# Kernel tuning notes

Measured on AMD Instinct MI355X. Metric: run time of the kernel, lower is better.

The kernel has to match this reference:

```python
import jax, jax.numpy as jnp
import numpy as np

D_MODEL = 128
N_HEADS = 8
RES_SCALE = 2.0 ** (-0.5)  # self_normalizing residual scale

OCC = np.array([65,66,67,68,69,70,71,72,73,74,75,76,77,81,82,83,84,88,89,90,94], dtype=np.int64)


def conv1d_same(x, w, groups=1):
    # x: [B, Cin, T], w: [Cout, Cin//groups, K] -> [B, Cout, T], 'same' padding, no bias
    return jax.lax.conv_general_dilated(
        x, w, window_strides=(1,), padding='SAME',
        dimension_numbers=('NCH', 'OIH', 'NCH'),
        feature_group_count=groups)


def setup_inputs() -> dict:
    key = jax.random.key(0)
    ks = jax.random.split(key, 7)
    B, C, T = 8, 128, 500
    L, D, O, K = 2, D_MODEL, 21, 9
    def lecun(k, shape, fan_in):
        return jax.random.normal(k, shape, dtype=jnp.float32) / jnp.sqrt(jnp.float32(fan_in))
    return {
        'x': jax.random.normal(ks[0], (B, C, T), dtype=jnp.float32),
        'occ_idx': jnp.asarray(OCC),
        'wq': lecun(ks[1], (L, D, O, K), O * K),
        'wk': lecun(ks[2], (L, C * D, 1, K), K),
        'wv': lecun(ks[3], (L, C * D, 1, K), K),
        'wproj': lecun(ks[4], (L, C, D), D),
        'w_head': lecun(ks[5], (40, C * T), C * T),
        'b_head': jnp.zeros((40,), dtype=jnp.float32),
    }


def reference(x, occ_idx, wq, wk, wv, wproj, w_head, b_head):
    B, C, T = x.shape
    L = wq.shape[0]
    H, D = N_HEADS, D_MODEL
    d = D // H  # head dim
    scale = d ** (-0.5)
    selu = jax.nn.selu
    for l in range(L):
        x_occ = x[:, occ_idx]                               # [B, O, T]
        Q = selu(conv1d_same(x_occ, wq[l]))                 # [B, D, T]
        K = selu(conv1d_same(x, wk[l], groups=C))           # [B, C*D, T]
        V = selu(conv1d_same(x, wv[l], groups=C))           # [B, C*D, T]
        Qh = Q.reshape(B, H, d, T)                          # b (h d) t -> b h d t
        Kh = K.reshape(B, C, H, d, T).transpose(0, 2, 1, 3, 4)  # b h c d t
        Vh = V.reshape(B, C, H, d, T).transpose(0, 2, 1, 3, 4)
        gates = selu(jnp.einsum('bhdt,bhcdt->bhct', Qh, Kh) * scale)
        out = jnp.einsum('bhct,bhcdt->bhcdt', gates, Vh)    # [B, H, C, d, T]
        out = out.transpose(0, 2, 1, 3, 4).reshape(B, C, D, T)  # b (c h d) t grouped by c
        # grouped 1x1 conv (groups=C): per-channel projection D -> 1
        out = selu(jnp.einsum('bcdt,cd->bct', out, wproj[l]))
        x = (x + out) * RES_SCALE
    logits = x.reshape(B, -1) @ w_head.T + b_head           # [B, n_classes]
    return logits
```

## Files before the change

kernel.cpp:

```cpp
#include <hip/hip_runtime.h>
#include <math.h>

#define T_LEN   500
#define C_CH    128
#define DM      128
#define N_OCC   21
#define KSZ     9
#define N_OUT   40
#define LOG2E   1.44269504088896340736f

typedef _Float16 f16x8 __attribute__((ext_vector_type(8)));
typedef float    f32x16 __attribute__((ext_vector_type(16)));

__device__ __forceinline__ float exp2_fast(float y) {
#if __has_builtin(__builtin_amdgcn_exp2f)
    return __builtin_amdgcn_exp2f(y);
#else
    return exp2f(y);
#endif
}

__device__ __forceinline__ float selu2(float y) {
    const float c1 = 0.7282904300f;
    const float la = 1.7580993408473766f;
    float e = exp2_fast(y);
    return y > 0.f ? c1 * y : fmaf(la, e, -la);
}

__global__ void wq_transpose(const float* __restrict__ wq, float* __restrict__ wqT) {
    int idx = blockIdx.x * 256 + threadIdx.x;
    if (idx >= 2 * N_OCC * KSZ * DM) return;
    int D  = idx & 127;
    int r  = idx >> 7;
    int k  = r % KSZ;
    int r2 = r / KSZ;
    int o  = r2 % N_OCC;
    int l  = r2 / N_OCC;
    wqT[idx] = wq[(((size_t)l * DM + D) * N_OCC + o) * KSZ + k] * LOG2E;
}

__global__ void wprep_kernel(const float* __restrict__ wk, const float* __restrict__ wv,
                             _Float16* __restrict__ wkh, _Float16* __restrict__ wvh)
{
    int idx = blockIdx.x * 256 + threadIdx.x;
    if (idx >= 2 * C_CH * 4 * 64) return;
    int lane = idx & 63;
    int ch   = (idx >> 6) & 3;
    int c    = (idx >> 8) & 127;
    int l    = idx >> 15;
    int tcol = lane & 31, hi = lane >> 5;
    int D    = ch * 32 + tcol;
    const float* wkp = wk + ((size_t)l * C_CH * DM + (size_t)c * DM + D) * KSZ;
    const float* wvp = wv + ((size_t)l * C_CH * DM + (size_t)c * DM + D) * KSZ;
#pragma unroll
    for (int j = 0; j < 8; ++j) {
        int k = 8 * hi + j;
        wkh[(size_t)idx * 8 + j] = (k < KSZ) ? (_Float16)(wkp[k] * LOG2E) : (_Float16)0.f;
        wvh[(size_t)idx * 8 + j] = (k < KSZ) ? (_Float16)(wvp[k] * LOG2E) : (_Float16)0.f;
    }
}

#define ATCH 4
__global__ __launch_bounds__(128) void qconv_kernel(
    const float* __restrict__ xin, const int* __restrict__ occ,
    const float* __restrict__ wqT, float* __restrict__ qtT2, int l)
{
    const int b  = blockIdx.y;
    const int t0 = blockIdx.x * ATCH;
    const int D  = threadIdx.x;
    __shared__ float xo[N_OCC][ATCH + 8];
    for (int i = threadIdx.x; i < N_OCC * (ATCH + 8); i += 128) {
        int o = i / (ATCH + 8), j = i % (ATCH + 8);
        int tg = t0 + j - 4;
        xo[o][j] = (tg >= 0 && tg < T_LEN)
                     ? xin[((size_t)b * C_CH + occ[o]) * T_LEN + tg] : 0.f;
    }
    __syncthreads();

    float acc[ATCH];
#pragma unroll
    for (int tt = 0; tt < ATCH; ++tt) acc[tt] = 0.f;

    for (int o = 0; o < N_OCC; ++o) {
        float xr[ATCH + 8];
#pragma unroll
        for (int j = 0; j < ATCH + 8; ++j) xr[j] = xo[o][j];
#pragma unroll
        for (int k = 0; k < KSZ; ++k) {
            float w = wqT[(((size_t)l * N_OCC + o) * KSZ + k) * DM + D];
#pragma unroll
            for (int tt = 0; tt < ATCH; ++tt)
                acc[tt] = fmaf(xr[tt + k], w, acc[tt]);
        }
    }
    float4 st;
#pragma unroll
    for (int tt = 0; tt < ATCH; ++tt) (&st.x)[tt] = selu2(acc[tt]);
    const int tile = t0 >> 5, tl = t0 & 31;
    *reinterpret_cast<float4*>(
        &qtT2[((size_t)(b * 16 + tile) * DM + D) * 32 + tl]) = st;
}

__global__ __launch_bounds__(256) void fused_layer(
    const float* __restrict__ xin, const float* __restrict__ qtT2,
    const f16x8* __restrict__ wkh, const f16x8* __restrict__ wvh,
    const float* __restrict__ wproj, float* __restrict__ xout, int l)
{
    const int c = blockIdx.x, b = blockIdx.y, zi = blockIdx.z;
    const int tid  = threadIdx.x;
    const int wave = tid >> 6;
    const int lane = tid & 63;
    const int tcol = lane & 31;
    const int hi   = lane >> 5;

    __shared__ float xs[272];
    const float* xp = xin + ((size_t)(b * C_CH + c)) * T_LEN;
    for (int i = tid; i < 272; i += 256) {
        int tg = zi * 256 + i - 4;
        xs[i] = (tg >= 0 && tg < T_LEN) ? xp[tg] : 0.f;
    }
    __syncthreads();

    const f16x8* wkf = wkh + ((size_t)(l * C_CH + c) * 4) * 64 + lane;
    const f16x8* wvf = wvh + ((size_t)(l * C_CH + c) * 4) * 64 + lane;
    f16x8 ak[4], av[4];
#pragma unroll
    for (int ch = 0; ch < 4; ++ch) {
        ak[ch] = wkf[ch * 64];
        av[ch] = wvf[ch * 64];
    }

    const float4* wp4p = reinterpret_cast<const float4*>(
        wproj + ((size_t)l * C_CH + c) * DM);

#pragma unroll 1
    for (int ti = 0; ti < 2; ++ti) {
        const int loc0 = wave * 64 + ti * 32;
        const int tile = zi * 8 + wave * 2 + ti;
        const int t    = zi * 256 + loc0 + tcol;

        f16x8 bfr;
        {
            const int base = loc0 + tcol + 8 * hi;
#pragma unroll
            for (int j = 0; j < 8; ++j) bfr[j] = (_Float16)xs[base + j];
        }

        float qk[8];
#pragma unroll
        for (int h = 0; h < 8; ++h) qk[h] = 0.f;

#pragma unroll
        for (int ch = 0; ch < 4; ++ch) {
            const float* qTp = qtT2
                + ((size_t)(b * 16 + tile) * DM + ch * 32 + 4 * hi) * 32 + tcol;
            float qv[16];
#pragma unroll
            for (int I = 0; I < 4; ++I)
#pragma unroll
                for (int i2 = 0; i2 < 4; ++i2)
                    qv[4 * I + i2] = qTp[(8 * I + i2) * 32];

            f32x16 acc;
#pragma unroll
            for (int j = 0; j < 16; ++j) acc[j] = 0.f;
            acc = __builtin_amdgcn_mfma_f32_32x32x16_f16(ak[ch], bfr, acc, 0, 0, 0);

            float pA = 0.f, pB = 0.f;
#pragma unroll
            for (int I = 0; I < 4; ++I) {
#pragma unroll
                for (int i2 = 0; i2 < 4; ++i2) {
                    float kv = selu2(acc[4 * I + i2]);
                    float qvv = qv[4 * I + i2];
                    if (I < 2) pA = fmaf(qvv, kv, pA);
                    else       pB = fmaf(qvv, kv, pB);
                }
            }
            qk[ch * 2 + 0] += pA;
            qk[ch * 2 + 1] += pB;
        }

        float g[8];
#pragma unroll
        for (int h = 0; h < 8; ++h) {
            float full = qk[h] + __shfl_xor(qk[h], 32);
            g[h] = selu2(full * (0.25f * LOG2E));
        }

        float outp = 0.f;
#pragma unroll
        for (int ch = 0; ch < 4; ++ch) {
            f32x16 acc;
#pragma unroll
            for (int j = 0; j < 16; ++j) acc[j] = 0.f;
            acc = __builtin_amdgcn_mfma_f32_32x32x16_f16(av[ch], bfr, acc, 0, 0, 0);
            float sA = 0.f, sB = 0.f;
#pragma unroll
            for (int I = 0; I < 4; ++I) {
                float4 wq4 = wp4p[ch * 8 + 2 * I + hi];
#pragma unroll
                for (int i2 = 0; i2 < 4; ++i2) {
                    float vv = selu2(acc[4 * I + i2]);
                    if (I < 2) sA = fmaf((&wq4.x)[i2], vv, sA);
                    else       sB = fmaf((&wq4.x)[i2], vv, sB);
                }
            }
            outp = fmaf(g[ch * 2 + 0], sA, outp);
            outp = fmaf(g[ch * 2 + 1], sB, outp);
        }
        float outf = outp + __shfl_xor(outp, 32);

        if (hi == 0 && t < T_LEN) {
            const float rs = 0.70710678118654752f;
            xout[((size_t)(b * C_CH + c)) * T_LEN + t]
                = (xs[loc0 + tcol + 4] + selu2(outf * LOG2E)) * rs;
        }
    }
}

#define NCHUNK 8
#define CHUNK  (C_CH * T_LEN / NCHUNK)
__global__ __launch_bounds__(256) void head_partial(
    const float* __restrict__ x, const float* __restrict__ wh,
    float* __restrict__ part)
{
    const int o  = blockIdx.x;
    const int ch = blockIdx.y;
    const int base = ch * CHUNK;
    const float4* wp = reinterpret_cast<const float4*>(wh + (size_t)o * (C_CH * T_LEN) + base);

    float acc[8];
#pragma unroll
    for (int b = 0; b < 8; ++b) acc[b] = 0.f;

    for (int i = threadIdx.x; i < CHUNK / 4; i += 256) {
        float4 w4 = wp[i];
#pragma unroll
        for (int b = 0; b < 8; ++b) {
            float4 x4 = reinterpret_cast<const float4*>(
                x + (size_t)b * (C_CH * T_LEN) + base)[i];
            acc[b] = fmaf(x4.x, w4.x, acc[b]);
            acc[b] = fmaf(x4.y, w4.y, acc[b]);
            acc[b] = fmaf(x4.z, w4.z, acc[b]);
            acc[b] = fmaf(x4.w, w4.w, acc[b]);
        }
    }

#pragma unroll
    for (int b = 0; b < 8; ++b)
#pragma unroll
        for (int off = 32; off > 0; off >>= 1)
            acc[b] += __shfl_down(acc[b], off);

    __shared__ float red[4][8];
    const int lane = threadIdx.x & 63, wid = threadIdx.x >> 6;
    if (lane == 0)
#pragma unroll
        for (int b = 0; b < 8; ++b) red[wid][b] = acc[b];
    __syncthreads();
    if (threadIdx.x < 8) {
        int b = threadIdx.x;
        part[((size_t)o * NCHUNK + ch) * 8 + b]
            = red[0][b] + red[1][b] + red[2][b] + red[3][b];
    }
}

__global__ __launch_bounds__(320) void head_final(
    const float* __restrict__ part, const float* __restrict__ bh,
    float* __restrict__ out)
{
    int i = threadIdx.x;
    if (i >= N_OUT * 8) return;
    int o = i >> 3, b = i & 7;
    float s = bh[o];
#pragma unroll
    for (int ch = 0; ch < NCHUNK; ++ch)
        s += part[((size_t)o * NCHUNK + ch) * 8 + b];
    out[b * N_OUT + o] = s;
}

extern "C" void kernel_launch(void* const* d_in, const int* in_sizes, int n_in,
                              void* d_out, int out_size, void* d_ws, size_t ws_size,
                              hipStream_t stream) {
    const float* x     = (const float*)d_in[0];
    const int*   occ   = (const int*)  d_in[1];
    const float* wq    = (const float*)d_in[2];
    const float* wk    = (const float*)d_in[3];
    const float* wv    = (const float*)d_in[4];
    const float* wproj = (const float*)d_in[5];
    const float* wh    = (const float*)d_in[6];
    const float* bh    = (const float*)d_in[7];
    float* out = (float*)d_out;

    float* ws  = (float*)d_ws;
    float* wqT = ws;
    float* qtb = wqT + 2 * N_OCC * KSZ * DM;
    float* xb0 = qtb + (size_t)8 * 16 * DM * 32;
    float* xb1 = xb0 + (size_t)8 * C_CH * T_LEN;
    float* hp  = xb1 + (size_t)8 * C_CH * T_LEN;
    _Float16* wkh = (_Float16*)(hp + N_OUT * NCHUNK * 8);
    _Float16* wvh = wkh + (size_t)2 * C_CH * 4 * 64 * 8;

    wq_transpose<<<dim3(189), 256, 0, stream>>>(wq, wqT);
    wprep_kernel<<<dim3(256), 256, 0, stream>>>(wk, wv, wkh, wvh);

    qconv_kernel<<<dim3(125, 8), 128, 0, stream>>>(x, occ, wqT, qtb, 0);
    fused_layer <<<dim3(128, 8, 2), 256, 0, stream>>>(
        x, qtb, (const f16x8*)wkh, (const f16x8*)wvh, wproj, xb0, 0);

    qconv_kernel<<<dim3(125, 8), 128, 0, stream>>>(xb0, occ, wqT, qtb, 1);
    fused_layer <<<dim3(128, 8, 2), 256, 0, stream>>>(
        xb0, qtb, (const f16x8*)wkh, (const f16x8*)wvh, wproj, xb1, 1);

    head_partial<<<dim3(N_OUT, NCHUNK), 256, 0, stream>>>(xb1, wh, hp);
    head_final  <<<dim3(1), 320, 0, stream>>>(hp, bh, out);
}
```

Measured before the change: 129.0 us.

## Repack Q layout for float4 loads, pre-pack fp16 x pairs, merge prep kernels

Changes the Q buffer layout written by the Q-conv kernel so the fused layer loads Q values as float4 vectors instead of 16 strided scalars. Builds a shared-memory array of packed fp16 x pairs so each MFMA B operand takes 4 LDS reads instead of 8 reads plus conversions. Merges the two weight-prep kernels into one launch and adds an occupancy hint to launch_bounds. The cost is an extra shared buffer and barrier, plus scattered 4-byte stores in the Q-conv kernel.

```diff
diff --git a/kernel.cpp b/kernel.cpp
--- a/kernel.cpp
+++ b/kernel.cpp
@@ -10,7 +10,10 @@
 #define LOG2E   1.44269504088896340736f
 
 typedef _Float16 f16x8 __attribute__((ext_vector_type(8)));
+typedef _Float16 f16x2 __attribute__((ext_vector_type(2)));
 typedef float    f32x16 __attribute__((ext_vector_type(16)));
+
+union pair_u { unsigned int u; f16x2 h; };
 
 __device__ __forceinline__ float exp2_fast(float y) {
 #if __has_builtin(__builtin_amdgcn_exp2f)
@@ -27,43 +30,43 @@
     return y > 0.f ? c1 * y : fmaf(la, e, -la);
 }
 
-__global__ void wq_transpose(const float* __restrict__ wq, float* __restrict__ wqT) {
+__global__ void prep_kernel(const float* __restrict__ wq,
+                            const float* __restrict__ wk, const float* __restrict__ wv,
+                            float* __restrict__ wqT,
+                            _Float16* __restrict__ wkh, _Float16* __restrict__ wvh)
+{
     int idx = blockIdx.x * 256 + threadIdx.x;
-    if (idx >= 2 * N_OCC * KSZ * DM) return;
-    int D  = idx & 127;
-    int r  = idx >> 7;
-    int k  = r % KSZ;
-    int r2 = r / KSZ;
-    int o  = r2 % N_OCC;
-    int l  = r2 / N_OCC;
-    wqT[idx] = wq[(((size_t)l * DM + D) * N_OCC + o) * KSZ + k] * LOG2E;
-}
-
-__global__ void wprep_kernel(const float* __restrict__ wk, const float* __restrict__ wv,
-                             _Float16* __restrict__ wkh, _Float16* __restrict__ wvh)
-{
-    int idx = blockIdx.x * 256 + threadIdx.x;
-    if (idx >= 2 * C_CH * 4 * 64) return;
-    int lane = idx & 63;
-    int ch   = (idx >> 6) & 3;
-    int c    = (idx >> 8) & 127;
-    int l    = idx >> 15;
-    int tcol = lane & 31, hi = lane >> 5;
-    int D    = ch * 32 + tcol;
-    const float* wkp = wk + ((size_t)l * C_CH * DM + (size_t)c * DM + D) * KSZ;
-    const float* wvp = wv + ((size_t)l * C_CH * DM + (size_t)c * DM + D) * KSZ;
-#pragma unroll
-    for (int j = 0; j < 8; ++j) {
-        int k = 8 * hi + j;
-        wkh[(size_t)idx * 8 + j] = (k < KSZ) ? (_Float16)(wkp[k] * LOG2E) : (_Float16)0.f;
-        wvh[(size_t)idx * 8 + j] = (k < KSZ) ? (_Float16)(wvp[k] * LOG2E) : (_Float16)0.f;
+    if (idx < 2 * N_OCC * KSZ * DM) {
+        int D  = idx & 127;
+        int r  = idx >> 7;
+        int k  = r % KSZ;
+        int r2 = r / KSZ;
+        int o  = r2 % N_OCC;
+        int l  = r2 / N_OCC;
+        wqT[idx] = wq[(((size_t)l * DM + D) * N_OCC + o) * KSZ + k] * LOG2E;
+    }
+    if (idx < 2 * C_CH * 4 * 64) {
+        int lane = idx & 63;
+        int ch   = (idx >> 6) & 3;
+        int c    = (idx >> 8) & 127;
+        int l    = idx >> 15;
+        int tcol = lane & 31, hi = lane >> 5;
+        int D    = ch * 32 + tcol;
+        const float* wkp = wk + ((size_t)l * C_CH * DM + (size_t)c * DM + D) * KSZ;
+        const float* wvp = wv + ((size_t)l * C_CH * DM + (size_t)c * DM + D) * KSZ;
+#pragma unroll
+        for (int j = 0; j < 8; ++j) {
+            int k = 8 * hi + j;
+            wkh[(size_t)idx * 8 + j] = (k < KSZ) ? (_Float16)(wkp[k] * LOG2E) : (_Float16)0.f;
+            wvh[(size_t)idx * 8 + j] = (k < KSZ) ? (_Float16)(wvp[k] * LOG2E) : (_Float16)0.f;
+        }
     }
 }
 
 #define ATCH 4
 __global__ __launch_bounds__(128) void qconv_kernel(
     const float* __restrict__ xin, const int* __restrict__ occ,
-    const float* __restrict__ wqT, float* __restrict__ qtT2, int l)
+    const float* __restrict__ wqT, float* __restrict__ qtP, int l)
 {
     const int b  = blockIdx.y;
     const int t0 = blockIdx.x * ATCH;
@@ -93,16 +96,17 @@
                 acc[tt] = fmaf(xr[tt + k], w, acc[tt]);
         }
     }
-    float4 st;
-#pragma unroll
-    for (int tt = 0; tt < ATCH; ++tt) (&st.x)[tt] = selu2(acc[tt]);
     const int tile = t0 >> 5, tl = t0 & 31;
-    *reinterpret_cast<float4*>(
-        &qtT2[((size_t)(b * 16 + tile) * DM + D) * 32 + tl]) = st;
-}
-
-__global__ __launch_bounds__(256) void fused_layer(
-    const float* __restrict__ xin, const float* __restrict__ qtT2,
+    const int ch = D >> 5, w = D & 31;
+    const int g  = 2 * (w >> 3) + ((w >> 2) & 1);
+    const int i2 = w & 3;
+    float* qb = qtP + ((((size_t)(b * 16 + tile) * 4 + ch) * 8 + g) * 32 + tl) * 4 + i2;
+#pragma unroll
+    for (int tt = 0; tt < ATCH; ++tt) qb[tt * 4] = selu2(acc[tt]);
+}
+
+__global__ __launch_bounds__(256, 4) void fused_layer(
+    const float* __restrict__ xin, const float* __restrict__ qtP,
     const f16x8* __restrict__ wkh, const f16x8* __restrict__ wvh,
     const float* __restrict__ wproj, float* __restrict__ xout, int l)
 {
@@ -114,10 +118,18 @@
     const int hi   = lane >> 5;
 
     __shared__ float xs[272];
+    __shared__ unsigned int xs2[271];
     const float* xp = xin + ((size_t)(b * C_CH + c)) * T_LEN;
     for (int i = tid; i < 272; i += 256) {
         int tg = zi * 256 + i - 4;
         xs[i] = (tg >= 0 && tg < T_LEN) ? xp[tg] : 0.f;
+    }
+    __syncthreads();
+    for (int i = tid; i < 271; i += 256) {
+        pair_u p;
+        p.h[0] = (_Float16)xs[i];
+        p.h[1] = (_Float16)xs[i + 1];
+        xs2[i] = p.u;
     }
     __syncthreads();
 
@@ -143,7 +155,11 @@
         {
             const int base = loc0 + tcol + 8 * hi;
 #pragma unroll
-            for (int j = 0; j < 8; ++j) bfr[j] = (_Float16)xs[base + j];
+            for (int j = 0; j < 4; ++j) {
+                pair_u p; p.u = xs2[base + 2 * j];
+                bfr[2 * j]     = p.h[0];
+                bfr[2 * j + 1] = p.h[1];
+            }
         }
 
         float qk[8];
@@ -152,14 +168,12 @@
 
 #pragma unroll
         for (int ch = 0; ch < 4; ++ch) {
-            const float* qTp = qtT2
-                + ((size_t)(b * 16 + tile) * DM + ch * 32 + 4 * hi) * 32 + tcol;
-            float qv[16];
+            const float4* qp = reinterpret_cast<const float4*>(qtP)
+                + (((size_t)(b * 16 + tile) * 4 + ch) * 8) * 32 + tcol;
+            float4 qv4[4];
 #pragma unroll
             for (int I = 0; I < 4; ++I)
-#pragma unroll
-                for (int i2 = 0; i2 < 4; ++i2)
-                    qv[4 * I + i2] = qTp[(8 * I + i2) * 32];
+                qv4[I] = qp[(2 * I + hi) * 32];
 
             f32x16 acc;
 #pragma unroll
@@ -172,7 +186,7 @@
 #pragma unroll
                 for (int i2 = 0; i2 < 4; ++i2) {
                     float kv = selu2(acc[4 * I + i2]);
-                    float qvv = qv[4 * I + i2];
+                    float qvv = (&qv4[I].x)[i2];
                     if (I < 2) pA = fmaf(qvv, kv, pA);
                     else       pB = fmaf(qvv, kv, pB);
                 }
@@ -302,8 +316,7 @@
     _Float16* wkh = (_Float16*)(hp + N_OUT * NCHUNK * 8);
     _Float16* wvh = wkh + (size_t)2 * C_CH * 4 * 64 * 8;
 
-    wq_transpose<<<dim3(189), 256, 0, stream>>>(wq, wqT);
-    wprep_kernel<<<dim3(256), 256, 0, stream>>>(wk, wv, wkh, wvh);
+    prep_kernel<<<dim3(256), 256, 0, stream>>>(wq, wk, wv, wqT, wkh, wvh);
 
     qconv_kernel<<<dim3(125, 8), 128, 0, stream>>>(x, occ, wqT, qtb, 0);
     fused_layer <<<dim3(128, 8, 2), 256, 0, stream>>>(
```

After: 398.0 us. 209% more time.
